# Performance work log

Measured on AMD Instinct MI355X. Metric: run time of the kernel, lower is better.

The kernel has to match this reference:

```python
import jax, jax.numpy as jnp
import numpy as np

B, N, E, H = 16, 196, 512, 8   # batch, tokens(14x14), embedding_channels(=KV_size_S), heads
HD = E // H                    # 64  spatial-attn head dim
C = 4 * E                      # 2048 = KV_size (concat of 4 branches)
HDC = C // H                   # 256 channel-attn (SelfAttentionTAT) head dim

def _ln(x, g, b, eps=1e-6):
    m = jnp.mean(x, -1, keepdims=True)
    v = jnp.mean(jnp.square(x - m), -1, keepdims=True)
    return (x - m) * jax.lax.rsqrt(v + eps) * g + b

def setup_inputs():
    key = jax.random.key(0)
    ks = jax.random.split(key, 16)
    n = lambda k, s, sc=0.02: jax.random.normal(k, s, jnp.float32) * sc
    return {
        "emb1": jax.random.normal(ks[0], (B, N, E), jnp.float32),
        "emb2": jax.random.normal(ks[1], (B, N, E), jnp.float32),
        "emb3": jax.random.normal(ks[2], (B, N, E), jnp.float32),
        "emb4": jax.random.normal(ks[3], (B, N, E), jnp.float32),
        "ln_attn_g": jnp.ones((4, E), jnp.float32), "ln_attn_b": jnp.zeros((4, E), jnp.float32),
        "lnC_g": jnp.ones((C,), jnp.float32), "lnC_b": jnp.zeros((C,), jnp.float32),
        "Wq_c": n(ks[4], (C, C)), "Wk_c": n(ks[5], (C, C)),
        "Wv_c": n(ks[6], (C, C)), "Wo_c": n(ks[7], (C, C)),
        "q_w": n(ks[8], (4, N, N), 0.05),              # query1..4 stacked (token-mixing Linear(196,196))
        "k_w": n(ks[9], (4 * N, 4 * N)),               # key   Linear(784,784)
        "v_w": n(ks[10], (4 * N, 4 * N)),              # value Linear(784,784)
        "out_w": n(ks[11], (4, E, E)),                 # out1..4 stacked
        "ln_ffn_g": jnp.ones((4, E), jnp.float32), "ln_ffn_b": jnp.zeros((4, E), jnp.float32),
        "fc1_w": n(ks[12], (4, E, 4 * E)), "fc1_b": n(ks[13], (4, 4 * E), 1e-6),
        "fc2_w": n(ks[14], (4, 4 * E, E)), "fc2_b": n(ks[15], (4, E), 1e-6),
    }

def reference(emb1, emb2, emb3, emb4, ln_attn_g, ln_attn_b, lnC_g, lnC_b,
              Wq_c, Wk_c, Wv_c, Wo_c, q_w, k_w, v_w, out_w,
              ln_ffn_g, ln_ffn_b, fc1_w, fc1_b, fc2_w, fc2_b):
    embs = jnp.stack([emb1, emb2, emb3, emb4])                         # [4,B,N,E]
    cx = _ln(embs, ln_attn_g[:, None, None, :], ln_attn_b[:, None, None, :])
    ec = _ln(jnp.concatenate([emb1, emb2, emb3, emb4], -1), lnC_g, lnC_b)  # [B,N,C]
    # SelfAttentionTAT: multi-head self-attention over the concatenated channel embedding
    q = (ec @ Wq_c).reshape(B, N, H, HDC).transpose(0, 2, 1, 3)
    k = (ec @ Wk_c).reshape(B, N, H, HDC).transpose(0, 2, 1, 3)
    v = (ec @ Wv_c).reshape(B, N, H, HDC).transpose(0, 2, 1, 3)
    s = jax.nn.softmax(jnp.einsum('bhnd,bhmd->bhnm', q, k) * np.float32(1.0 / np.sqrt(HDC)), -1)
    T_hat = jnp.einsum('bhnm,bhmd->bhnd', s, v).transpose(0, 2, 1, 3).reshape(B, N, C) @ Wo_c
    # split channel dim into 4 chunks, concat along token axis -> [B,4N,E]
    KV_S = T_hat.reshape(B, N, 4, E).transpose(0, 2, 1, 3).reshape(B, 4 * N, E)
    # token-mixing projections (Linear applied to the token axis)
    Q = jnp.einsum('gbnc,gnm->gbmc', cx, q_w)                          # [4,B,N,E]
    K = jnp.einsum('bnc,nm->bmc', KV_S, k_w)                           # [B,4N,E]
    V = jnp.einsum('bnc,nm->bmc', KV_S, v_w)
    Qh = Q.reshape(4, B, N, H, HD).transpose(0, 1, 3, 2, 4)            # [4,B,H,N,HD]
    Kh = K.reshape(B, 4 * N, H, HD).transpose(0, 2, 1, 3)              # [B,H,4N,HD]
    Vh = V.reshape(B, 4 * N, H, HD).transpose(0, 2, 1, 3)
    attn = jnp.einsum('gbhnd,bhmd->gbhnm', Qh, Kh)                     # [4,B,H,N,4N]
    # InstanceNorm2d (no affine, eps=1e-5) over (N,4N) per (branch,batch,head) instead of 1/sqrt(d)
    m = jnp.mean(attn, (-2, -1), keepdims=True)
    var = jnp.mean(jnp.square(attn - m), (-2, -1), keepdims=True)
    p = jax.nn.softmax((attn - m) * jax.lax.rsqrt(var + 1e-5), -1)
    ctx = jnp.einsum('gbhnm,bhmd->gbhnd', p, Vh)                       # [4,B,H,N,HD]
    # faithful to source: only branch 1 is permuted before .view; branches 2-4
    # are .view'ed directly from [B,H,N,HD] (head-major flatten)
    c1 = ctx[0].transpose(0, 2, 1, 3).reshape(B, N, E)
    crest = ctx[1:].reshape(3, B, N, E)
    cmerged = jnp.concatenate([c1[None], crest], 0)                    # [4,B,N,E]
    h = embs + jnp.einsum('gbne,gef->gbnf', cmerged, out_w)            # residual 1
    x = _ln(h, ln_ffn_g[:, None, None, :], ln_ffn_b[:, None, None, :])
    x = jax.nn.gelu(jnp.einsum('gbne,gef->gbnf', x, fc1_w) + fc1_b[:, None, None, :], approximate=False)
    x = jnp.einsum('gbnf,gfe->gbne', x, fc2_w) + fc2_b[:, None, None, :]
    out = x + h                                                        # residual 2
    return (out[0], out[1], out[2], out[3])
```

## Files before the change

### kernel.cpp

```cpp
#include <hip/hip_runtime.h>
#include <hip/hip_bf16.h>
#include <math.h>

typedef __hip_bfloat16 bf16;
typedef __attribute__((ext_vector_type(8))) short v8s;
typedef __attribute__((ext_vector_type(4))) short v4s;
typedef __attribute__((ext_vector_type(4))) float v4f;

#define Bq   16
#define Nq   196
#define Eq   512
#define Hq   8
#define HDq  64
#define Cq   2048
#define HDCq 256
#define N4q  784
#define BNq  (Bq*Nq)
#define SLOT ((long)BNq*Cq)
#define L2E  1.44269504f

__global__ __launch_bounds__(256) void k_fill(float* __restrict__ out, long n, float v) {
  long i = (long)blockIdx.x * 256 + threadIdx.x;
  if (i < n) out[i] = v;
}

__device__ __forceinline__ float blk_sum(float v, float* buf) {
  #pragma unroll
  for (int off = 32; off; off >>= 1) v += __shfl_down(v, off, 64);
  int tid = threadIdx.x;
  __syncthreads();
  if ((tid & 63) == 0) buf[tid >> 6] = v;
  __syncthreads();
  return buf[0] + buf[1] + buf[2] + buf[3];
}

__device__ __forceinline__ float blk_max(float v, float* buf) {
  #pragma unroll
  for (int off = 32; off; off >>= 1) v = fmaxf(v, __shfl_down(v, off, 64));
  int tid = threadIdx.x;
  __syncthreads();
  if ((tid & 63) == 0) buf[tid >> 6] = v;
  __syncthreads();
  return fmaxf(fmaxf(buf[0], buf[1]), fmaxf(buf[2], buf[3]));
}

__device__ __forceinline__ unsigned int pack2bf(float a, float b) {
  unsigned short ha = __builtin_bit_cast(unsigned short, (bf16)a);
  unsigned short hb = __builtin_bit_cast(unsigned short, (bf16)b);
  return (unsigned int)ha | ((unsigned int)hb << 16);
}

__global__ __launch_bounds__(256) void k_ln_concat(
    const float* __restrict__ e1, const float* __restrict__ e2,
    const float* __restrict__ e3, const float* __restrict__ e4,
    const float* __restrict__ gamma, const float* __restrict__ beta,
    bf16* __restrict__ ec) {
  __shared__ float buf[4];
  int row = blockIdx.x;
  int tid = threadIdx.x;
  float vals[8];
  #pragma unroll
  for (int i = 0; i < 8; i++) {
    const float* src = (i < 2) ? e1 : (i < 4) ? e2 : (i < 6) ? e3 : e4;
    vals[i] = src[(long)row * Eq + (i & 1) * 256 + tid];
  }
  float s = 0;
  #pragma unroll
  for (int i = 0; i < 8; i++) s += vals[i];
  float mean = blk_sum(s, buf) * (1.f / 2048.f);
  float ss = 0;
  #pragma unroll
  for (int i = 0; i < 8; i++) { float d = vals[i] - mean; ss += d * d; }
  float rstd = rsqrtf(blk_sum(ss, buf) * (1.f / 2048.f) + 1e-6f);
  #pragma unroll
  for (int i = 0; i < 8; i++) {
    int c = tid + i * 256;
    ec[(long)row * Cq + c] = (bf16)((vals[i] - mean) * rstd * gamma[c] + beta[c]);
  }
}

__global__ __launch_bounds__(256) void k_ln_branch(
    const float* __restrict__ e1, const float* __restrict__ e2,
    const float* __restrict__ e3, const float* __restrict__ e4,
    const float* __restrict__ gamma, const float* __restrict__ beta,
    bf16* __restrict__ cx) {
  __shared__ float buf[4];
  int idx = blockIdx.x;
  int tid = threadIdx.x;
  int row = idx % BNq; int g = idx / BNq;
  const float* src = (g == 0) ? e1 : (g == 1) ? e2 : (g == 2) ? e3 : e4;
  float v0 = src[(long)row * Eq + tid];
  float v1 = src[(long)row * Eq + 256 + tid];
  float mean = blk_sum(v0 + v1, buf) * (1.f / 512.f);
  float d0 = v0 - mean, d1 = v1 - mean;
  float var = blk_sum(d0 * d0 + d1 * d1, buf) * (1.f / 512.f);
  float rstd = rsqrtf(var + 1e-6f);
  cx[(long)idx * Eq + tid]       = (bf16)(d0 * rstd * gamma[g * Eq + tid]       + beta[g * Eq + tid]);
  cx[(long)idx * Eq + 256 + tid] = (bf16)(d1 * rstd * gamma[g * Eq + 256 + tid] + beta[g * Eq + 256 + tid]);
}

__global__ __launch_bounds__(256) void k_ln_rows(
    const bf16* __restrict__ x, const float* __restrict__ gamma, const float* __restrict__ beta,
    bf16* __restrict__ out) {
  __shared__ float buf[4];
  int idx = blockIdx.x;
  int tid = threadIdx.x;
  int g = idx / BNq;
  float v0 = (float)x[(long)idx * Eq + tid];
  float v1 = (float)x[(long)idx * Eq + 256 + tid];
  float mean = blk_sum(v0 + v1, buf) * (1.f / 512.f);
  float d0 = v0 - mean, d1 = v1 - mean;
  float var = blk_sum(d0 * d0 + d1 * d1, buf) * (1.f / 512.f);
  float rstd = rsqrtf(var + 1e-6f);
  out[(long)idx * Eq + tid]       = (bf16)(d0 * rstd * gamma[g * Eq + tid]       + beta[g * Eq + tid]);
  out[(long)idx * Eq + 256 + tid] = (bf16)(d1 * rstd * gamma[g * Eq + 256 + tid] + beta[g * Eq + 256 + tid]);
}

template<bool HAS_BIAS, bool GELU, int RES_MODE, bool OUT_F32>
__global__ __launch_bounds__(256, 2) void k_gemm(
    const bf16* __restrict__ A, const float* __restrict__ W,
    const float* __restrict__ bias, const void* __restrict__ res,
    void* __restrict__ out, int M, int Nn, int K) {
  __shared__ short As[256][76];
  __shared__ short Bs[64][72];
  int tid = threadIdx.x;
  int l = tid & 63, w = tid >> 6;
  int li = l & 15, lg = l >> 4;
  int m0 = blockIdx.x * 256, n0 = blockIdx.y * 64;

  v4f acc[4][4] = {};

  int ar = tid >> 1, ak = (tid & 1) * 32;
  long arow0 = (long)m0 + ar;       if (arow0 >= M) arow0 = M - 1;
  long arow1 = (long)m0 + ar + 128; if (arow1 >= M) arow1 = M - 1;
  const short* ap0 = (const short*)A + arow0 * K + ak;
  const short* ap1 = (const short*)A + arow1 * K + ak;

  for (int k0 = 0; k0 < K; k0 += 64) {
    {
      const short* p0 = ap0 + k0;
      const short* p1 = ap1 + k0;
      *(v8s*)&As[ar][ak]            = *(const v8s*)p0;
      *(v8s*)&As[ar][ak + 8]        = *(const v8s*)(p0 + 8);
      *(v8s*)&As[ar][ak + 16]       = *(const v8s*)(p0 + 16);
      *(v8s*)&As[ar][ak + 24]       = *(const v8s*)(p0 + 24);
      *(v8s*)&As[ar + 128][ak]      = *(const v8s*)p1;
      *(v8s*)&As[ar + 128][ak + 8]  = *(const v8s*)(p1 + 8);
      *(v8s*)&As[ar + 128][ak + 16] = *(const v8s*)(p1 + 16);
      *(v8s*)&As[ar + 128][ak + 24] = *(const v8s*)(p1 + 24);
    }
    #pragma unroll
    for (int t = 0; t < 2; t++) {
      int p = tid + 256 * t;
      int kp = p >> 4, nf = p & 15;
      const float* wp = W + (long)(k0 + 2 * kp) * Nn + n0 + nf * 4;
      float4 w0 = *(const float4*)wp;
      float4 w1 = *(const float4*)(wp + Nn);
      float f0[4] = {w0.x, w0.y, w0.z, w0.w};
      float f1[4] = {w1.x, w1.y, w1.z, w1.w};
      int ko = (2 * kp) ^ ((nf & 7) << 3);
      #pragma unroll
      for (int e = 0; e < 4; e++)
        *(unsigned int*)&Bs[nf * 4 + e][ko] = pack2bf(f0[e], f1[e]);
    }
    __syncthreads();
    #pragma unroll
    for (int ks = 0; ks < 2; ks++) {
      v8s af[4], bfr[4];
      #pragma unroll
      for (int mi = 0; mi < 4; mi++)
        af[mi] = *(const v8s*)&As[w * 64 + mi * 16 + li][ks * 32 + lg * 8];
      #pragma unroll
      for (int nj = 0; nj < 4; nj++) {
        int rn = nj * 16 + li;
        int ko = (ks * 32 + lg * 8) ^ (((rn >> 2) & 7) << 3);
        bfr[nj] = *(const v8s*)&Bs[rn][ko];
      }
      #pragma unroll
      for (int mi = 0; mi < 4; mi++)
        #pragma unroll
        for (int nj = 0; nj < 4; nj++)
          acc[mi][nj] = __builtin_amdgcn_mfma_f32_16x16x32_bf16(af[mi], bfr[nj], acc[mi][nj], 0, 0, 0);
    }
    __syncthreads();
  }

  #pragma unroll
  for (int nj = 0; nj < 4; nj++) {
    int n = n0 + nj * 16 + li;
    float bv = HAS_BIAS ? bias[n] : 0.f;
    #pragma unroll
    for (int mi = 0; mi < 4; mi++) {
      #pragma unroll
      for (int rr = 0; rr < 4; rr++) {
        int m = m0 + w * 64 + mi * 16 + lg * 4 + rr;
        if (m < M) {
          float x = acc[mi][nj][rr] + bv;
          if (GELU) x = 0.5f * x * (1.f + erff(x * 0.70710678118f));
          if (RES_MODE == 1) x += ((const float*)res)[(long)m * Nn + n];
          if (RES_MODE == 2) x += (float)((const bf16*)res)[(long)m * Nn + n];
          if (OUT_F32) ((float*)out)[(long)m * Nn + n] = x;
          else         ((bf16*)out)[(long)m * Nn + n] = (bf16)x;
        }
      }
    }
  }
}

template<bool REINDEX, bool TRANSV>
__global__ __launch_bounds__(256) void k_mix_mfma(
    const bf16* __restrict__ X, const float* __restrict__ Wt, bf16* __restrict__ out,
    int T) {
  __shared__ short Aws[128][72];
  __shared__ short Xs[128][72];
  int tid = threadIdx.x;
  int l = tid & 63, w = tid >> 6;
  int li = l & 15, lg = l >> 4;
  int wr = w >> 1, wc = w & 1;
  int bidx = blockIdx.x;
  int c0 = blockIdx.y * 128;
  int m0 = blockIdx.z * 128;
  const float* W = REINDEX ? Wt : (Wt + (long)(bidx >> 4) * T * T);
  const short* xb = (const short*)X + (REINDEX ? (long)bidx * Nq * Cq
                                               : (long)bidx * Nq * Eq);
  bf16* ob = out + (long)bidx * T * Eq;

  v4f acc[4][4] = {};
  int nsteps = (T + 63) / 64;
  bool mfull = (m0 + 128 <= T);
  for (int s = 0; s < nsteps; s++) {
    int k0 = s * 64;
    if (mfull) {
      #pragma unroll
      for (int t = 0; t < 4; t++) {
        int p = tid + 256 * t;
        int kp = p >> 5, mf = p & 31;
        int n0r = k0 + 2 * kp; if (n0r > T - 1) n0r = T - 1;
        int n1r = k0 + 2 * kp + 1; if (n1r > T - 1) n1r = T - 1;
        const float* w0p = W + (long)n0r * T + m0 + mf * 4;
        const float* w1p = W + (long)n1r * T + m0 + mf * 4;
        float4 w0 = *(const float4*)w0p;
        float4 w1 = *(const float4*)w1p;
        float f0[4] = {w0.x, w0.y, w0.z, w0.w};
        float f1[4] = {w1.x, w1.y, w1.z, w1.w};
        int ko = (2 * kp) ^ ((mf & 7) << 3);
        #pragma unroll
        for (int e = 0; e < 4; e++)
          *(unsigned int*)&Aws[mf * 4 + e][ko] = pack2bf(f0[e], f1[e]);
      }
    } else {
      #pragma unroll
      for (int t = 0; t < 4; t++) {
        int p = tid + 256 * t;
        int kp = p >> 5, mf = p & 31;
        int n0r = min(k0 + 2 * kp, T - 1);
        int n1r = min(k0 + 2 * kp + 1, T - 1);
        int ko = (2 * kp) ^ ((mf & 7) << 3);
        #pragma unroll
        for (int e = 0; e < 4; e++) {
          int m = min(m0 + mf * 4 + e, T - 1);
          *(unsigned int*)&Aws[mf * 4 + e][ko] =
              pack2bf(W[(long)n0r * T + m], W[(long)n1r * T + m]);
        }
      }
    }
    #pragma unroll
    for (int t = 0; t < 2; t++) {
      int p = tid + 256 * t;
      int np = p >> 4, cg = p & 15;
      int n0r = k0 + 2 * np, n1r = n0r + 1;
      v8s x0 = {}, x1 = {};
      if (n0r < T) {
        const short* xp;
        if (REINDEX) {
          int q4 = (n0r >= 588) ? 3 : (n0r >= 392) ? 2 : (n0r >= 196) ? 1 : 0;
          xp = xb + (long)(n0r - q4 * Nq) * Cq + q4 * Eq + c0 + cg * 8;
        } else {
          xp = xb + (long)n0r * Eq + c0 + cg * 8;
        }
        x0 = *(const v8s*)xp;
      }
      if (n1r < T) {
        const short* xp;
        if (REINDEX) {
          int q4 = (n1r >= 588) ? 3 : (n1r >= 392) ? 2 : (n1r >= 196) ? 1 : 0;
          xp = xb + (long)(n1r - q4 * Nq) * Cq + q4 * Eq + c0 + cg * 8;
        } else {
          xp = xb + (long)n1r * Eq + c0 + cg * 8;
        }
        x1 = *(const v8s*)xp;
      }
      int ko = (2 * np) ^ ((cg & 7) << 3);
      #pragma unroll
      for (int e = 0; e < 8; e++) {
        unsigned short h0 = (unsigned short)x0[e];
        unsigned short h1 = (unsigned short)x1[e];
        *(unsigned int*)&Xs[cg * 8 + e][ko] = (unsigned int)h0 | ((unsigned int)h1 << 16);
      }
    }
    __syncthreads();
    #pragma unroll
    for (int ks = 0; ks < 2; ks++) {
      v8s af[4], bfr[4];
      #pragma unroll
      for (int mi = 0; mi < 4; mi++) {
        int rm = wr * 64 + mi * 16 + li;
        int ko = (ks * 32 + lg * 8) ^ (((rm >> 2) & 7) << 3);
        af[mi] = *(const v8s*)&Aws[rm][ko];
      }
      #pragma unroll
      for (int nj = 0; nj < 4; nj++) {
        int rc = wc * 64 + nj * 16 + li;
        int ko = (ks * 32 + lg * 8) ^ (((rc >> 3) & 7) << 3);
        bfr[nj] = *(const v8s*)&Xs[rc][ko];
      }
      if (TRANSV) {
        #pragma unroll
        for (int nj = 0; nj < 4; nj++)
          #pragma unroll
          for (int mi = 0; mi < 4; mi++)
            acc[nj][mi] = __builtin_amdgcn_mfma_f32_16x16x32_bf16(bfr[nj], af[mi], acc[nj][mi], 0, 0, 0);
      } else {
        #pragma unroll
        for (int mi = 0; mi < 4; mi++)
          #pragma unroll
          for (int nj = 0; nj < 4; nj++)
            acc[mi][nj] = __builtin_amdgcn_mfma_f32_16x16x32_bf16(af[mi], bfr[nj], acc[mi][nj], 0, 0, 0);
      }
    }
    __syncthreads();
  }

  if (TRANSV) {
    bf16* obt = out + (long)bidx * Eq * T;
    #pragma unroll
    for (int mi = 0; mi < 4; mi++) {
      int m = m0 + wr * 64 + mi * 16 + li;
      if (m < T) {
        #pragma unroll
        for (int nj = 0; nj < 4; nj++) {
          #pragma unroll
          for (int rr = 0; rr < 4; rr++) {
            int c = c0 + wc * 64 + nj * 16 + lg * 4 + rr;
            obt[(long)c * T + m] = (bf16)acc[nj][mi][rr];
          }
        }
      }
    }
  } else {
    #pragma unroll
    for (int nj = 0; nj < 4; nj++) {
      int c = c0 + wc * 64 + nj * 16 + li;
      #pragma unroll
      for (int mi = 0; mi < 4; mi++) {
        #pragma unroll
        for (int rr = 0; rr < 4; rr++) {
          int m = m0 + wr * 64 + mi * 16 + lg * 4 + rr;
          if (m < T) ob[(long)m * Eq + c] = (bf16)acc[mi][nj][rr];
        }
      }
    }
  }
}

__global__ __launch_bounds__(256) void k_chan_attn(
    const bf16* __restrict__ q, const bf16* __restrict__ k, const bf16* __restrict__ v,
    bf16* __restrict__ T) {
  __shared__ short P[16 * 232];
  __shared__ float mbuf[4][16];
  __shared__ float dbuf[4][16];
  int tid = threadIdx.x;
  int l = tid & 63, w = tid >> 6;
  int bid = blockIdx.x;
  int it = bid / 128, bh = bid % 128;
  int h = bh & 7; int b = bh >> 3;
  int i0 = it * 16;
  int li = l & 15, lg = l >> 4;

  for (int z = tid; z < 16 * 28; z += 256) P[(z / 28) * 232 + 196 + (z % 28)] = 0;

  int arow = i0 + li;
  const short* qp = (const short*)(q + ((long)(b * Nq) + (arow < Nq ? arow : 0)) * Cq + h * HDCq + lg * 8);
  v8s qf[8] = {};
  if (arow < Nq) {
    #pragma unroll
    for (int kk = 0; kk < 8; kk++) qf[kk] = *(const v8s*)(qp + kk * 32);
  }

  float accS[4][4];
  float lmax[4] = {-1e30f, -1e30f, -1e30f, -1e30f};
  #pragma unroll
  for (int jj = 0; jj < 4; jj++) {
    int jt = w + jj * 4;
    if (jt < 13) {
      int jrow = jt * 16 + li;
      int jr = jrow < Nq ? jrow : Nq - 1;
      const short* kp = (const short*)(k + ((long)(b * Nq) + jr) * Cq + h * HDCq + lg * 8);
      v4f acc = {0.f, 0.f, 0.f, 0.f};
      #pragma unroll
      for (int kk = 0; kk < 8; kk++) {
        v8s kf = *(const v8s*)(kp + kk * 32);
        acc = __builtin_amdgcn_mfma_f32_16x16x32_bf16(qf[kk], kf, acc, 0, 0, 0);
      }
      bool valid = jrow < Nq;
      #pragma unroll
      for (int rr = 0; rr < 4; rr++) {
        float s = acc[rr] * (0.0625f * L2E);
        accS[jj][rr] = s;
        if (valid) lmax[rr] = fmaxf(lmax[rr], s);
      }
    } else {
      #pragma unroll
      for (int rr = 0; rr < 4; rr++) accS[jj][rr] = 0.f;
    }
  }
  #pragma unroll
  for (int rr = 0; rr < 4; rr++) {
    float mv = lmax[rr];
    #pragma unroll
    for (int m = 1; m < 16; m <<= 1) mv = fmaxf(mv, __shfl_xor(mv, m, 64));
    if (li == 0) mbuf[w][lg * 4 + rr] = mv;
  }
  __syncthreads();
  float gmx[4];
  #pragma unroll
  for (int rr = 0; rr < 4; rr++) {
    int row = lg * 4 + rr;
    gmx[rr] = fmaxf(fmaxf(mbuf[0][row], mbuf[1][row]), fmaxf(mbuf[2][row], mbuf[3][row]));
  }

  float ds4[4] = {0.f, 0.f, 0.f, 0.f};
  #pragma unroll
  for (int jj = 0; jj < 4; jj++) {
    int jt = w + jj * 4;
    if (jt < 13) {
      int jrow = jt * 16 + li;
      bool valid = jrow < Nq;
      #pragma unroll
      for (int rr = 0; rr < 4; rr++) {
        float e = valid ? exp2f(accS[jj][rr] - gmx[rr]) : 0.f;
        bf16 pb = (bf16)e;
        ds4[rr] += (float)pb;
        P[(lg * 4 + rr) * 232 + jt * 16 + li] = __builtin_bit_cast(short, pb);
      }
    }
  }
  #pragma unroll
  for (int rr = 0; rr < 4; rr++) {
    float sv = ds4[rr];
    #pragma unroll
    for (int m = 1; m < 16; m <<= 1) sv += __shfl_xor(sv, m, 64);
    if (li == 0) dbuf[w][lg * 4 + rr] = sv;
  }
  __syncthreads();

  v8s pfs[7];
  #pragma unroll
  for (int js = 0; js < 7; js++) pfs[js] = *(const v8s*)&P[li * 232 + js * 32 + lg * 8];

  const short* vbase = (const short*)(v + (long)(b * Nq) * Cq + h * HDCq);
  float accO[4][4];
  #pragma unroll
  for (int dt = 0; dt < 4; dt++) {
    int d = w * 64 + dt * 16 + li;
    v4f acc = {0.f, 0.f, 0.f, 0.f};
    #pragma unroll
    for (int js = 0; js < 6; js++) {
      const short* vp = vbase + (long)(js * 32 + lg * 8) * Cq + d;
      v8s vf;
      #pragma unroll
      for (int e = 0; e < 8; e++) vf[e] = vp[(long)e * Cq];
      acc = __builtin_amdgcn_mfma_f32_16x16x32_bf16(vf, pfs[js], acc, 0, 0, 0);
    }
    {
      int j0 = 192 + lg * 8;
      const short* vp = vbase + (long)j0 * Cq + d;
      v8s vf = {};
      #pragma unroll
      for (int e = 0; e < 8; e++) if (j0 + e < Nq) vf[e] = vp[(long)e * Cq];
      acc = __builtin_amdgcn_mfma_f32_16x16x32_bf16(vf, pfs[6], acc, 0, 0, 0);
    }
    #pragma unroll
    for (int rr = 0; rr < 4; rr++) accO[dt][rr] = acc[rr];
  }

  float inv = 1.f / (dbuf[0][li] + dbuf[1][li] + dbuf[2][li] + dbuf[3][li]);
  int ic = i0 + li;
  if (ic < Nq) {
    #pragma unroll
    for (int dt = 0; dt < 4; dt++) {
      bf16* tp = T + ((long)(b * Nq) + ic) * Cq + h * HDCq + w * 64 + dt * 16 + lg * 4;
      v4s ov;
      #pragma unroll
      for (int rr = 0; rr < 4; rr++) {
        bf16 t = (bf16)(accO[dt][rr] * inv);
        ov[rr] = __builtin_bit_cast(short, t);
      }
      *(v4s*)tp = ov;
    }
  }
}

__global__ __launch_bounds__(256) void k_gram(
    const bf16* __restrict__ Qs, const bf16* __restrict__ Ks,
    float* __restrict__ G, float* __restrict__ XS) {
  __shared__ short XT[64][136];
  int tid = threadIdx.x;
  int l = tid & 63, w = tid >> 6;
  int li = l & 15, lg = l >> 4;
  int r = blockIdx.x;
  const short* xb; int R;
  if (r < 512) {
    int gb = r >> 3, h = r & 7;
    xb = (const short*)Qs + (long)gb * Nq * Eq + h * 64; R = Nq;
  } else {
    int idx = r - 512; int b = idx >> 3, h = idx & 7;
    xb = (const short*)Ks + (long)b * N4q * Eq + h * 64; R = N4q;
  }
  v4f acc[4] = {};
  float xsum = 0.f;
  for (int n0 = 0; n0 < R; n0 += 128) {
    __syncthreads();
    #pragma unroll
    for (int t = 0; t < 4; t++) {
      int task = tid + 256 * t;
      int nn = task >> 3, oct = task & 7;
      int n = n0 + nn;
      v8s xv = {};
      if (n < R) xv = *(const v8s*)(xb + (long)n * Eq + oct * 8);
      #pragma unroll
      for (int e = 0; e < 8; e++) XT[oct * 8 + e][nn] = xv[e];
    }
    __syncthreads();
    if (tid < 64) {
      #pragma unroll
      for (int c = 0; c < 128; c += 8) {
        v8s v = *(const v8s*)&XT[tid][c];
        #pragma unroll
        for (int e = 0; e < 8; e++) xsum += (float)__builtin_bit_cast(bf16, v[e]);
      }
    }
    #pragma unroll
    for (int ks = 0; ks < 4; ks++) {
      v8s af = *(const v8s*)&XT[w * 16 + li][ks * 32 + lg * 8];
      #pragma unroll
      for (int t2 = 0; t2 < 4; t2++) {
        v8s bf2 = *(const v8s*)&XT[t2 * 16 + li][ks * 32 + lg * 8];
        acc[t2] = __builtin_amdgcn_mfma_f32_16x16x32_bf16(af, bf2, acc[t2], 0, 0, 0);
      }
    }
  }
  float* gout = G + (long)r * 4096;
  #pragma unroll
  for (int t2 = 0; t2 < 4; t2++)
    #pragma unroll
    for (int rr = 0; rr < 4; rr++)
      gout[(w * 16 + lg * 4 + rr) * 64 + t2 * 16 + li] = acc[t2][rr];
  if (tid < 64) XS[(long)r * 64 + tid] = xsum;
}

__global__ __launch_bounds__(256) void k_statfin(
    const float* __restrict__ G, const float* __restrict__ XS,
    float* __restrict__ stat) {
  __shared__ float buf[4];
  int r = blockIdx.x;
  int h = r & 7; int b = (r >> 3) & 15;
  int kidx = 512 + b * 8 + h;
  const float* gq = G + (long)r * 4096;
  const float* gk = G + (long)kidx * 4096;
  int tid = threadIdx.x;
  float f = 0.f;
  for (int i = tid; i < 4096; i += 256) f += gq[i] * gk[i];
  float frob = blk_sum(f, buf);
  float md = (tid < 64) ? XS[(long)r * 64 + tid] * XS[(long)kidx * 64 + tid] : 0.f;
  float meandot = blk_sum(md, buf);
  if (tid == 0) {
    float inv = 1.f / ((float)Nq * (float)N4q);
    float mean = meandot * inv;
    float var = frob * inv - mean * mean;
    stat[1024 + r * 2] = mean;
    stat[1024 + r * 2 + 1] = rsqrtf(var + 1e-5f);
  }
}

__global__ __launch_bounds__(256) void k_spa_attn(
    const bf16* __restrict__ Q, const bf16* __restrict__ K, const bf16* __restrict__ VT,
    const float* __restrict__ stat, bf16* __restrict__ ctx) {
  __shared__ short P[16 * 808];
  __shared__ float mbuf[4][16];
  __shared__ float dbuf[4][16];
  int tid = threadIdx.x;
  int l = tid & 63, w = tid >> 6;
  int bid = blockIdx.x;
  int it = bid / 512, r = bid % 512;
  int h = r & 7; int gb = r >> 3; int b = gb & 15;
  int i0 = it * 16;
  int li = l & 15, lg = l >> 4;

  for (int z = tid; z < 16 * 24; z += 256) P[(z / 24) * 808 + 784 + (z % 24)] = 0;

  float rstdl2 = stat[1024 + r * 2 + 1] * L2E;

  int arow = i0 + li;
  const short* qp = (const short*)(Q + ((long)gb * Nq + (arow < Nq ? arow : 0)) * Eq + h * 64 + lg * 8);
  v8s qf0 = {}, qf1 = {};
  if (arow < Nq) { qf0 = *(const v8s*)qp; qf1 = *(const v8s*)(qp + 32); }

  const short* kbase = (const short*)(K + ((long)b * N4q + li) * Eq + h * 64 + lg * 8);

  float accS[13][4];
  float lmax = -1e30f;
  #pragma unroll
  for (int jj = 0; jj < 13; jj++) {
    int jt = w + jj * 4;
    if (jt < 49) {
      const short* kp = kbase + (long)jt * 16 * Eq;
      v8s kf0 = *(const v8s*)kp;
      v8s kf1 = *(const v8s*)(kp + 32);
      v4f acc = {0.f, 0.f, 0.f, 0.f};
      acc = __builtin_amdgcn_mfma_f32_16x16x32_bf16(kf0, qf0, acc, 0, 0, 0);
      acc = __builtin_amdgcn_mfma_f32_16x16x32_bf16(kf1, qf1, acc, 0, 0, 0);
      #pragma unroll
      for (int rr = 0; rr < 4; rr++) {
        accS[jj][rr] = acc[rr];
        lmax = fmaxf(lmax, acc[rr]);
      }
    } else {
      #pragma unroll
      for (int rr = 0; rr < 4; rr++) accS[jj][rr] = 0.f;
    }
  }
  lmax = fmaxf(lmax, __shfl_xor(lmax, 16, 64));
  lmax = fmaxf(lmax, __shfl_xor(lmax, 32, 64));
  if (lg == 0) mbuf[w][li] = lmax;
  __syncthreads();
  float gmx = fmaxf(fmaxf(mbuf[0][li], mbuf[1][li]), fmaxf(mbuf[2][li], mbuf[3][li]));

  float dsum = 0.f;
  #pragma unroll
  for (int jj = 0; jj < 13; jj++) {
    int jt = w + jj * 4;
    if (jt < 49) {
      v4s pk;
      #pragma unroll
      for (int rr = 0; rr < 4; rr++) {
        float e = exp2f((accS[jj][rr] - gmx) * rstdl2);
        bf16 pb = (bf16)e;
        dsum += (float)pb;
        pk[rr] = __builtin_bit_cast(short, pb);
      }
      *(v4s*)&P[li * 808 + jt * 16 + lg * 4] = pk;
    }
  }
  dsum += __shfl_xor(dsum, 16, 64);
  dsum += __shfl_xor(dsum, 32, 64);
  if (lg == 0) dbuf[w][li] = dsum;
  __syncthreads();

  const short* vtb = (const short*)VT + ((long)b * Eq + h * 64 + w * 16 + li) * N4q;
  v4f accO = {0.f, 0.f, 0.f, 0.f};
  for (int js = 0; js < 24; js++) {
    v8s vf = *(const v8s*)(vtb + js * 32 + lg * 8);
    v8s pf = *(const v8s*)&P[li * 808 + js * 32 + lg * 8];
    accO = __builtin_amdgcn_mfma_f32_16x16x32_bf16(vf, pf, accO, 0, 0, 0);
  }
  {
    int jb = 768 + lg * 8;
    v8s vf = {};
    if (jb < N4q) vf = *(const v8s*)(vtb + jb);
    v8s pf = *(const v8s*)&P[li * 808 + 768 + lg * 8];
    accO = __builtin_amdgcn_mfma_f32_16x16x32_bf16(vf, pf, accO, 0, 0, 0);
  }
  float inv = 1.f / (dbuf[0][li] + dbuf[1][li] + dbuf[2][li] + dbuf[3][li]);
  int ic = i0 + li;
  if (ic < Nq) {
    bf16* cp = ctx + (long)r * Nq * 64 + (long)ic * 64 + w * 16 + lg * 4;
    v4s ov;
    #pragma unroll
    for (int rr = 0; rr < 4; rr++) {
      bf16 t = (bf16)(accO[rr] * inv);
      ov[rr] = __builtin_bit_cast(short, t);
    }
    *(v4s*)cp = ov;
  }
}

__global__ __launch_bounds__(256) void k_scramble(
    const bf16* __restrict__ ctx, bf16* __restrict__ cm) {
  long i = (long)blockIdx.x * 256 + threadIdx.x;
  int e = (int)(i & 511); long t = i >> 9;
  int n = (int)(t % Nq); long gb = t / Nq;
  int g = (int)(gb >> 4);
  long srcIdx;
  if (g == 0) {
    int h = e >> 6, d = e & 63;
    srcIdx = ((gb * 8 + h) * (long)Nq + n) * 64 + d;
  } else {
    int l = n * 512 + e;
    int h = l / 12544; int rem = l % 12544; int n2 = rem >> 6; int d = rem & 63;
    srcIdx = ((gb * 8 + h) * (long)Nq + n2) * 64 + d;
  }
  cm[i] = ctx[srcIdx];
}

extern "C" void kernel_launch(void* const* d_in, const int* in_sizes, int n_in,
                              void* d_out, int out_size, void* d_ws, size_t ws_size,
                              hipStream_t stream) {
  const int expect[22] = {
    1605632, 1605632, 1605632, 1605632,
    2048, 2048, 2048, 2048,
    4194304, 4194304, 4194304, 4194304,
    153664, 614656, 614656, 1048576,
    2048, 2048,
    4194304, 8192, 4194304, 2048
  };
  long fillBlocks = ((long)out_size + 255) / 256;
  if (n_in != 22) {
    k_fill<<<fillBlocks, 256, 0, stream>>>((float*)d_out, out_size, 3000.f);
    return;
  }
  for (int i = 0; i < 22; i++) {
    if (in_sizes[i] != expect[i]) {
      k_fill<<<fillBlocks, 256, 0, stream>>>((float*)d_out, out_size, 1000.f + 20.f * i);
      return;
    }
  }

  const float* e1 = (const float*)d_in[0];
  const float* e2 = (const float*)d_in[1];
  const float* e3 = (const float*)d_in[2];
  const float* e4 = (const float*)d_in[3];
  const float* ln_attn_g = (const float*)d_in[4];
  const float* ln_attn_b = (const float*)d_in[5];
  const float* lnC_g = (const float*)d_in[6];
  const float* lnC_b = (const float*)d_in[7];
  const float* Wq = (const float*)d_in[8];
  const float* Wk = (const float*)d_in[9];
  const float* Wv = (const float*)d_in[10];
  const float* Wo = (const float*)d_in[11];
  const float* q_w = (const float*)d_in[12];
  const float* k_w = (const float*)d_in[13];
  const float* v_w = (const float*)d_in[14];
  const float* out_w = (const float*)d_in[15];
  const float* ln_ffn_g = (const float*)d_in[16];
  const float* ln_ffn_b = (const float*)d_in[17];
  const float* fc1_w = (const float*)d_in[18];
  const float* fc1_b = (const float*)d_in[19];
  const float* fc2_w = (const float*)d_in[20];
  const float* fc2_b = (const float*)d_in[21];

  bf16* W0 = (bf16*)d_ws;
  bf16* W1 = W0 + SLOT;
  bf16* W2 = W0 + 2 * SLOT;
  bf16* OUTS = (bf16*)d_out;
  float* OUT = (float*)d_out;
  float* ST = (float*)((char*)d_ws + 3 * SLOT * sizeof(bf16));
  float* GR = OUT + SLOT / 2;
  float* XSUM = GR + 640 * 4096;

  dim3 gqkv(13, Cq / 64);
  long off = (long)BNq * Eq;

  k_ln_concat<<<BNq, 256, 0, stream>>>(e1, e2, e3, e4, lnC_g, lnC_b, W0);
  k_gemm<false,false,0,false><<<gqkv, 256, 0, stream>>>(W0, Wq, nullptr, nullptr, W1, BNq, Cq, Cq);
  k_gemm<false,false,0,false><<<gqkv, 256, 0, stream>>>(W0, Wk, nullptr, nullptr, W2, BNq, Cq, Cq);
  k_gemm<false,false,0,false><<<gqkv, 256, 0, stream>>>(W0, Wv, nullptr, nullptr, OUTS, BNq, Cq, Cq);
  k_chan_attn<<<Bq * Hq * 13, 256, 0, stream>>>(W1, W2, OUTS, W0);
  k_gemm<false,false,0,false><<<gqkv, 256, 0, stream>>>(W0, Wo, nullptr, nullptr, W1, BNq, Cq, Cq);

  k_ln_branch<<<4 * BNq, 256, 0, stream>>>(e1, e2, e3, e4, ln_attn_g, ln_attn_b, W0);
  dim3 gmq(64, 4, 2);
  k_mix_mfma<false,false><<<gmq, 256, 0, stream>>>(W0, q_w, W2, Nq);
  dim3 gmkv(16, 4, 7);
  k_mix_mfma<true,false><<<gmkv, 256, 0, stream>>>(W1, k_w, OUTS, N4q);
  k_mix_mfma<true,true><<<gmkv, 256, 0, stream>>>(W1, v_w, W0, N4q);

  k_gram<<<640, 256, 0, stream>>>(W2, OUTS, GR, XSUM);
  k_statfin<<<512, 256, 0, stream>>>(GR, XSUM, ST);
  k_spa_attn<<<512 * 13, 256, 0, stream>>>(W2, OUTS, W0, ST, W1);

  k_scramble<<<(4L * BNq * Eq) / 256, 256, 0, stream>>>(W1, W2);
  dim3 gh(13, Eq / 64);
  const float* embp[4] = {e1, e2, e3, e4};
  for (int g = 0; g < 4; g++)
    k_gemm<false,false,1,false><<<gh, 256, 0, stream>>>(
        W2 + g * off, out_w + (long)g * Eq * Eq, nullptr, embp[g], W0 + g * off, BNq, Eq, Eq);

  k_ln_rows<<<4 * BNq, 256, 0, stream>>>(W0, ln_ffn_g, ln_ffn_b, W1);
  dim3 gfc1(13, (4 * Eq) / 64);
  dim3 gfc2(13, Eq / 64);
  for (int g = 0; g < 4; g++) {
    k_gemm<true,true,0,false><<<gfc1, 256, 0, stream>>>(
        W1 + g * off, fc1_w + (long)g * Eq * 4 * Eq, fc1_b + (long)g * 4 * Eq, nullptr,
        W2, BNq, 4 * Eq, Eq);
    k_gemm<true,false,2,true><<<gfc2, 256, 0, stream>>>(
        W2, fc2_w + (long)g * 4 * Eq * Eq, fc2_b + (long)g * Eq, W0 + g * off,
        OUT + g * off, BNq, Eq, 4 * Eq);
  }
}
```

Before: 1.240 ms.

## Pre-transpose weights to bf16, batch out-proj GEMMs, swizzle attention P buffer

Adds a kernel that converts fp32 weights to transposed bf16 and a GEMM variant that reads these pre-transposed bf16 weights with vectorized loads. It is used for the four channel-attention projections and for a batched out-projection over all four branches in one launch, replacing the loop of four launches. The spatial attention P scratch in shared memory now uses an XOR swizzle to cut LDS bank conflicts. Each call pays for the extra conversion kernels and the weight-buffer traffic, and the WB scratch space overlaps the output region used for the Gram buffer.

```diff
diff --git a/kernel.cpp b/kernel.cpp
--- a/kernel.cpp
+++ b/kernel.cpp
@@ -19,6 +19,8 @@
 #define SLOT ((long)BNq*Cq)
 #define L2E  1.44269504f
 
+struct P4 { const void* p[4]; };
+
 __global__ __launch_bounds__(256) void k_fill(float* __restrict__ out, long n, float v) {
   long i = (long)blockIdx.x * 256 + threadIdx.x;
   if (i < n) out[i] = v;
@@ -32,16 +34,6 @@
   if ((tid & 63) == 0) buf[tid >> 6] = v;
   __syncthreads();
   return buf[0] + buf[1] + buf[2] + buf[3];
-}
-
-__device__ __forceinline__ float blk_max(float v, float* buf) {
-  #pragma unroll
-  for (int off = 32; off; off >>= 1) v = fmaxf(v, __shfl_down(v, off, 64));
-  int tid = threadIdx.x;
-  __syncthreads();
-  if ((tid & 63) == 0) buf[tid >> 6] = v;
-  __syncthreads();
-  return fmaxf(fmaxf(buf[0], buf[1]), fmaxf(buf[2], buf[3]));
 }
 
 __device__ __forceinline__ unsigned int pack2bf(float a, float b) {
@@ -114,6 +106,110 @@
   float rstd = rsqrtf(var + 1e-6f);
   out[(long)idx * Eq + tid]       = (bf16)(d0 * rstd * gamma[g * Eq + tid]       + beta[g * Eq + tid]);
   out[(long)idx * Eq + 256 + tid] = (bf16)(d1 * rstd * gamma[g * Eq + 256 + tid] + beta[g * Eq + 256 + tid]);
+}
+
+__global__ __launch_bounds__(256) void k_cvt_t(
+    const float* __restrict__ W, bf16* __restrict__ WT, int K, int Nn) {
+  __shared__ short T[64][72];
+  int tid = threadIdx.x;
+  long zo = (long)blockIdx.z * K * Nn;
+  int n0 = blockIdx.x * 64, k0 = blockIdx.y * 64;
+  int r = tid >> 2, c = (tid & 3) * 16;
+  const float* src = W + zo + (long)(k0 + r) * Nn + n0 + c;
+  float4 f0 = *(const float4*)src;
+  float4 f1 = *(const float4*)(src + 4);
+  float4 f2 = *(const float4*)(src + 8);
+  float4 f3 = *(const float4*)(src + 12);
+  float fv[16] = {f0.x,f0.y,f0.z,f0.w, f1.x,f1.y,f1.z,f1.w,
+                  f2.x,f2.y,f2.z,f2.w, f3.x,f3.y,f3.z,f3.w};
+  #pragma unroll
+  for (int e = 0; e < 16; e++)
+    T[c + e][r] = __builtin_bit_cast(short, (bf16)fv[e]);
+  __syncthreads();
+  short* dst = (short*)WT + zo + (long)(n0 + r) * K + k0 + c;
+  *(v8s*)dst       = *(const v8s*)&T[r][c];
+  *(v8s*)(dst + 8) = *(const v8s*)&T[r][c + 8];
+}
+
+template<bool HAS_BIAS, bool GELU, int RES_MODE, bool OUT_F32>
+__global__ __launch_bounds__(256, 2) void k_gemm_bt(
+    const bf16* __restrict__ A, const bf16* __restrict__ WT,
+    const float* __restrict__ bias, P4 resp,
+    void* __restrict__ out, int M, int Nn, int K,
+    long aStride, long wStride, long oStride) {
+  __shared__ short As[256][76];
+  __shared__ short Bs[64][76];
+  int tid = threadIdx.x;
+  int l = tid & 63, w = tid >> 6;
+  int li = l & 15, lg = l >> 4;
+  int z = blockIdx.z;
+  int m0 = blockIdx.x * 256, n0 = blockIdx.y * 64;
+  const short* Ab = (const short*)A + (long)z * aStride;
+  const short* Wb = (const short*)WT + (long)z * wStride;
+  const void* res = resp.p[z];
+
+  v4f acc[4][4] = {};
+
+  int ar = tid >> 1, ak = (tid & 1) * 32;
+  long arow0 = (long)m0 + ar;       if (arow0 >= M) arow0 = M - 1;
+  long arow1 = (long)m0 + ar + 128; if (arow1 >= M) arow1 = M - 1;
+  const short* ap0 = Ab + arow0 * K + ak;
+  const short* ap1 = Ab + arow1 * K + ak;
+  int br = tid >> 2, bk = (tid & 3) * 16;
+  const short* bp = Wb + (long)(n0 + br) * K + bk;
+
+  for (int k0 = 0; k0 < K; k0 += 64) {
+    const short* p0 = ap0 + k0;
+    const short* p1 = ap1 + k0;
+    *(v8s*)&As[ar][ak]            = *(const v8s*)p0;
+    *(v8s*)&As[ar][ak + 8]        = *(const v8s*)(p0 + 8);
+    *(v8s*)&As[ar][ak + 16]       = *(const v8s*)(p0 + 16);
+    *(v8s*)&As[ar][ak + 24]       = *(const v8s*)(p0 + 24);
+    *(v8s*)&As[ar + 128][ak]      = *(const v8s*)p1;
+    *(v8s*)&As[ar + 128][ak + 8]  = *(const v8s*)(p1 + 8);
+    *(v8s*)&As[ar + 128][ak + 16] = *(const v8s*)(p1 + 16);
+    *(v8s*)&As[ar + 128][ak + 24] = *(const v8s*)(p1 + 24);
+    *(v8s*)&Bs[br][bk]            = *(const v8s*)(bp + k0);
+    *(v8s*)&Bs[br][bk + 8]        = *(const v8s*)(bp + k0 + 8);
+    __syncthreads();
+    #pragma unroll
+    for (int ks = 0; ks < 2; ks++) {
+      v8s af[4], bfr[4];
+      #pragma unroll
+      for (int mi = 0; mi < 4; mi++)
+        af[mi] = *(const v8s*)&As[w * 64 + mi * 16 + li][ks * 32 + lg * 8];
+      #pragma unroll
+      for (int nj = 0; nj < 4; nj++)
+        bfr[nj] = *(const v8s*)&Bs[nj * 16 + li][ks * 32 + lg * 8];
+      #pragma unroll
+      for (int mi = 0; mi < 4; mi++)
+        #pragma unroll
+        for (int nj = 0; nj < 4; nj++)
+          acc[mi][nj] = __builtin_amdgcn_mfma_f32_16x16x32_bf16(af[mi], bfr[nj], acc[mi][nj], 0, 0, 0);
+    }
+    __syncthreads();
+  }
+
+  #pragma unroll
+  for (int nj = 0; nj < 4; nj++) {
+    int n = n0 + nj * 16 + li;
+    float bv = HAS_BIAS ? bias[n] : 0.f;
+    #pragma unroll
+    for (int mi = 0; mi < 4; mi++) {
+      #pragma unroll
+      for (int rr = 0; rr < 4; rr++) {
+        int m = m0 + w * 64 + mi * 16 + lg * 4 + rr;
+        if (m < M) {
+          float x = acc[mi][nj][rr] + bv;
+          if (GELU) x = 0.5f * x * (1.f + erff(x * 0.70710678118f));
+          if (RES_MODE == 1) x += ((const float*)res)[(long)m * Nn + n];
+          if (RES_MODE == 2) x += (float)((const bf16*)res)[(long)m * Nn + n];
+          if (OUT_F32) (((float*)out) + (long)z * oStride)[(long)m * Nn + n] = x;
+          else         (((bf16*)out)  + (long)z * oStride)[(long)m * Nn + n] = (bf16)x;
+        }
+      }
+    }
+  }
 }
 
 template<bool HAS_BIAS, bool GELU, int RES_MODE, bool OUT_F32>
@@ -586,7 +682,7 @@
 __global__ __launch_bounds__(256) void k_spa_attn(
     const bf16* __restrict__ Q, const bf16* __restrict__ K, const bf16* __restrict__ VT,
     const float* __restrict__ stat, bf16* __restrict__ ctx) {
-  __shared__ short P[16 * 808];
+  __shared__ short P[16 * 832];
   __shared__ float mbuf[4][16];
   __shared__ float dbuf[4][16];
   int tid = threadIdx.x;
@@ -597,7 +693,10 @@
   int i0 = it * 16;
   int li = l & 15, lg = l >> 4;
 
-  for (int z = tid; z < 16 * 24; z += 256) P[(z / 24) * 808 + 784 + (z % 24)] = 0;
+  for (int z = tid; z < 16 * 48; z += 256) {
+    int i = z / 48, j = 784 + (z % 48);
+    P[i * 832 + ((((j >> 3) ^ (i & 7))) << 3) + (j & 7)] = 0;
+  }
 
   float rstdl2 = stat[1024 + r * 2 + 1] * L2E;
 
@@ -649,7 +748,7 @@
         dsum += (float)pb;
         pk[rr] = __builtin_bit_cast(short, pb);
       }
-      *(v4s*)&P[li * 808 + jt * 16 + lg * 4] = pk;
+      *(v4s*)&P[li * 832 + (((jt * 2 + (lg >> 1)) ^ (li & 7)) << 3) + ((lg & 1) << 2)] = pk;
     }
   }
   dsum += __shfl_xor(dsum, 16, 64);
@@ -661,14 +760,14 @@
   v4f accO = {0.f, 0.f, 0.f, 0.f};
   for (int js = 0; js < 24; js++) {
     v8s vf = *(const v8s*)(vtb + js * 32 + lg * 8);
-    v8s pf = *(const v8s*)&P[li * 808 + js * 32 + lg * 8];
+    v8s pf = *(const v8s*)&P[li * 832 + (((js * 4 + lg) ^ (li & 7)) << 3)];
     accO = __builtin_amdgcn_mfma_f32_16x16x32_bf16(vf, pf, accO, 0, 0, 0);
   }
   {
     int jb = 768 + lg * 8;
     v8s vf = {};
     if (jb < N4q) vf = *(const v8s*)(vtb + jb);
-    v8s pf = *(const v8s*)&P[li * 808 + 768 + lg * 8];
+    v8s pf = *(const v8s*)&P[li * 832 + (((96 + lg) ^ (li & 7)) << 3)];
     accO = __builtin_amdgcn_mfma_f32_16x16x32_bf16(vf, pf, accO, 0, 0, 0);
   }
   float inv = 1.f / (dbuf[0][li] + dbuf[1][li] + dbuf[2][li] + dbuf[3][li]);
@@ -757,16 +856,23 @@
   float* ST = (float*)((char*)d_ws + 3 * SLOT * sizeof(bf16));
   float* GR = OUT + SLOT / 2;
   float* XSUM = GR + 640 * 4096;
+  bf16* WB = (bf16*)(OUT + SLOT / 2);
 
   dim3 gqkv(13, Cq / 64);
+  dim3 gcvC(Cq / 64, Cq / 64);
   long off = (long)BNq * Eq;
+  P4 nores = {};
 
   k_ln_concat<<<BNq, 256, 0, stream>>>(e1, e2, e3, e4, lnC_g, lnC_b, W0);
-  k_gemm<false,false,0,false><<<gqkv, 256, 0, stream>>>(W0, Wq, nullptr, nullptr, W1, BNq, Cq, Cq);
-  k_gemm<false,false,0,false><<<gqkv, 256, 0, stream>>>(W0, Wk, nullptr, nullptr, W2, BNq, Cq, Cq);
-  k_gemm<false,false,0,false><<<gqkv, 256, 0, stream>>>(W0, Wv, nullptr, nullptr, OUTS, BNq, Cq, Cq);
+  k_cvt_t<<<gcvC, 256, 0, stream>>>(Wq, WB, Cq, Cq);
+  k_gemm_bt<false,false,0,false><<<gqkv, 256, 0, stream>>>(W0, WB, nullptr, nores, W1, BNq, Cq, Cq, 0, 0, 0);
+  k_cvt_t<<<gcvC, 256, 0, stream>>>(Wk, WB, Cq, Cq);
+  k_gemm_bt<false,false,0,false><<<gqkv, 256, 0, stream>>>(W0, WB, nullptr, nores, W2, BNq, Cq, Cq, 0, 0, 0);
+  k_cvt_t<<<gcvC, 256, 0, stream>>>(Wv, WB, Cq, Cq);
+  k_gemm_bt<false,false,0,false><<<gqkv, 256, 0, stream>>>(W0, WB, nullptr, nores, OUTS, BNq, Cq, Cq, 0, 0, 0);
   k_chan_attn<<<Bq * Hq * 13, 256, 0, stream>>>(W1, W2, OUTS, W0);
-  k_gemm<false,false,0,false><<<gqkv, 256, 0, stream>>>(W0, Wo, nullptr, nullptr, W1, BNq, Cq, Cq);
+  k_cvt_t<<<gcvC, 256, 0, stream>>>(Wo, WB, Cq, Cq);
+  k_gemm_bt<false,false,0,false><<<gqkv, 256, 0, stream>>>(W0, WB, nullptr, nores, W1, BNq, Cq, Cq, 0, 0, 0);
 
   k_ln_branch<<<4 * BNq, 256, 0, stream>>>(e1, e2, e3, e4, ln_attn_g, ln_attn_b, W0);
   dim3 gmq(64, 4, 2);
@@ -777,14 +883,13 @@
 
   k_gram<<<640, 256, 0, stream>>>(W2, OUTS, GR, XSUM);
   k_statfin<<<512, 256, 0, stream>>>(GR, XSUM, ST);
+  k_cvt_t<<<dim3(Eq / 64, Eq / 64, 4), 256, 0, stream>>>(out_w, WB, Eq, Eq);
   k_spa_attn<<<512 * 13, 256, 0, stream>>>(W2, OUTS, W0, ST, W1);
 
   k_scramble<<<(4L * BNq * Eq) / 256, 256, 0, stream>>>(W1, W2);
-  dim3 gh(13, Eq / 64);
-  const float* embp[4] = {e1, e2, e3, e4};
-  for (int g = 0; g < 4; g++)
-    k_gemm<false,false,1,false><<<gh, 256, 0, stream>>>(
-        W2 + g * off, out_w + (long)g * Eq * Eq, nullptr, embp[g], W0 + g * off, BNq, Eq, Eq);
+  P4 resp; resp.p[0] = e1; resp.p[1] = e2; resp.p[2] = e3; resp.p[3] = e4;
+  k_gemm_bt<false,false,1,false><<<dim3(13, Eq / 64, 4), 256, 0, stream>>>(
+      W2, WB, nullptr, resp, W0, BNq, Eq, Eq, off, (long)Eq * Eq, off);
 
   k_ln_rows<<<4 * BNq, 256, 0, stream>>>(W0, ln_ffn_g, ln_ffn_b, W1);
   dim3 gfc1(13, (4 * Eq) / 64);
```

Result: faster. 1.184 ms (-4.6%).
